# Kernel tuning notes

Measured on AMD Instinct MI355X. Metric: run time of the kernel, lower is better.

The kernel has to match this reference:

```python
import jax, jax.numpy as jnp
import numpy as np

N = 100000  # nodes
IN, HID, OUT = 64, 64, 32  # in_channels, 2*out_channels, out_channels
E = 1600000  # edges (avg degree 16)


def _gcn_conv(x, src, dst, deg_inv_sqrt, W, b, n):
    # PyG GCNConv: h = X W ; out[dst] += norm * h[src] ; out += b
    h = x @ W  # [N, F_out]
    norm = (deg_inv_sqrt[src] * deg_inv_sqrt[dst])[:, None]  # [E+N, 1]
    msg = h[src] * norm  # gathered edge messages [E+N, F_out]
    return jax.ops.segment_sum(msg, dst, num_segments=n) + b


def setup_inputs() -> dict:
    key = jax.random.key(0)
    ks = jax.random.split(key, 6)
    x = jax.random.normal(ks[0], (N, IN), dtype=jnp.float32)
    edge_index = jax.random.randint(ks[1], (2, E), 0, N, dtype=jnp.int32)
    # glorot-ish init for the two GCN layers
    W1 = jax.random.normal(ks[2], (IN, HID), dtype=jnp.float32) * (1.0 / np.sqrt(IN))
    b1 = jnp.zeros((HID,), dtype=jnp.float32)
    W2 = jax.random.normal(ks[3], (HID, OUT), dtype=jnp.float32) * (1.0 / np.sqrt(HID))
    b2 = jnp.zeros((OUT,), dtype=jnp.float32)
    return {"x": x, "edge_index": edge_index, "W1": W1, "b1": b1, "W2": W2, "b2": b2}


def reference(x, edge_index, W1, b1, W2, b2):
    n = x.shape[0]
    loop = jnp.arange(n, dtype=edge_index.dtype)
    src = jnp.concatenate([edge_index[0], loop])  # add self-loops
    dst = jnp.concatenate([edge_index[1], loop])
    # symmetric degree normalization (deg includes self-loops, so deg >= 1)
    deg = jax.ops.segment_sum(jnp.ones(dst.shape[0], x.dtype), dst, num_segments=n)
    dis = jax.lax.rsqrt(deg)
    h = jax.nn.relu(_gcn_conv(x, src, dst, dis, W1, b1, n))
    out = jax.nn.relu(_gcn_conv(h, src, dst, dis, W2, b2, n))
    return out
```

## Files before the change

### kernel.cpp

```cpp
#include <hip/hip_runtime.h>


#define NBMAX 512

__device__ __forceinline__ unsigned bf16pair(float a, float b) {
  unsigned ua = __float_as_uint(a), ub = __float_as_uint(b);
  ua = (ua + 0x7fffu + ((ua >> 16) & 1u)) >> 16;
  ub = (ub + 0x7fffu + ((ub >> 16) & 1u)) >> 16;
  return ua | (ub << 16);
}
__device__ __forceinline__ float bf_lo(unsigned v) { return __uint_as_float(v << 16); }
__device__ __forceinline__ float bf_hi(unsigned v) { return __uint_as_float(v & 0xffff0000u); }


__global__ __launch_bounds__(256) void k_coarsehist(const int* __restrict__ dst,
                                                    int* __restrict__ ch,
                                                    int E, int NB) {
  __shared__ int lh[NBMAX];
  int t = threadIdx.x;
  lh[t] = 0; lh[t + 256] = 0;
  __syncthreads();
  for (int e = blockIdx.x * 256 + t; e < E; e += gridDim.x * 256)
    atomicAdd(&lh[dst[e] >> 8], 1);
  __syncthreads();
  for (int b = t; b < NB; b += 256) {
    int c = lh[b];
    if (c) atomicAdd(&ch[b], c);
  }
}

__global__ __launch_bounds__(512) void k_scanb(const int* __restrict__ ch,
                                               int* __restrict__ cbase,
                                               int* __restrict__ gcur,
                                               int* __restrict__ off,
                                               int NB, int n, int E) {
  __shared__ int lds[512];
  int t = threadIdx.x;
  int v = (t < NB) ? ch[t] : 0;
  lds[t] = v;
  __syncthreads();
  for (int d = 1; d < 512; d <<= 1) {
    int u = (t >= d) ? lds[t - d] : 0;
    __syncthreads();
    lds[t] += u;
    __syncthreads();
  }
  if (t < NB) {
    int exc = lds[t] - v;
    cbase[t] = exc;
    gcur[t]  = exc;
  }
  if (t == 0) off[n] = E;
}

__global__ __launch_bounds__(256) void k_binpairs(const int* __restrict__ src,
                                                  const int* __restrict__ dst,
                                                  int* __restrict__ gcur,
                                                  unsigned* __restrict__ pairs,
                                                  int E, int NB) {
  __shared__ int lcnt[NBMAX], gbase[NBMAX];
  int t = threadIdx.x;
  int tile0 = blockIdx.x * 4096;
  lcnt[t] = 0; lcnt[t + 256] = 0;
  __syncthreads();
#pragma unroll
  for (int j = 0; j < 16; ++j) {
    int e = tile0 + j * 256 + t;
    if (e < E) atomicAdd(&lcnt[dst[e] >> 8], 1);
  }
  __syncthreads();
  for (int b = t; b < NB; b += 256) {
    int c = lcnt[b];
    if (c) gbase[b] = atomicAdd(&gcur[b], c);
    lcnt[b] = 0;
  }
  __syncthreads();
#pragma unroll
  for (int j = 0; j < 16; ++j) {
    int e = tile0 + j * 256 + t;
    if (e < E) {
      int dv = dst[e];
      int b  = dv >> 8;
      int slot = atomicAdd(&lcnt[b], 1);
      pairs[gbase[b] + slot] = ((unsigned)src[e] << 8) | (unsigned)(dv & 255);
    }
  }
}

__global__ __launch_bounds__(256) void k_finesort(const unsigned* __restrict__ pairs,
                                                  const int* __restrict__ ch,
                                                  const int* __restrict__ cbase,
                                                  int* __restrict__ off,
                                                  float* __restrict__ dis,
                                                  int* __restrict__ ssrc, int n) {
  __shared__ int hist[256], lcur[256], wsum[4];
  __shared__ int sbuf[8192];
  int b = blockIdx.x;
  int node0 = b << 8;
  int nn = min(256, n - node0);
  int cnt = ch[b], base = cbase[b];
  int t = threadIdx.x;
  hist[t] = 0;
  __syncthreads();
  for (int e = t; e < cnt; e += 256)
    atomicAdd(&hist[pairs[base + e] & 255u], 1);
  __syncthreads();
  int c = hist[t];
  int lane = t & 63, wv = t >> 6;
  int inc = c;
#pragma unroll
  for (int d = 1; d < 64; d <<= 1) {
    int u = __shfl_up(inc, d);
    if (lane >= d) inc += u;
  }
  if (lane == 63) wsum[wv] = inc;
  __syncthreads();
  int pre = 0;
  for (int w = 0; w < wv; ++w) pre += wsum[w];
  int exc = pre + inc - c;
  if (t < nn) {
    off[node0 + t] = base + exc;
    dis[node0 + t] = rsqrtf((float)(c + 1));
  }
  lcur[t] = exc;
  __syncthreads();
  bool inlds = (cnt <= 8192);
  for (int e = t; e < cnt; e += 256) {
    unsigned p = pairs[base + e];
    int slot = atomicAdd(&lcur[p & 255u], 1);
    int sv = (int)(p >> 8);
    if (inlds) sbuf[slot] = sv;
    else       ssrc[base + slot] = sv;
  }
  __syncthreads();
  if (inlds)
    for (int e = t; e < cnt; e += 256) ssrc[base + e] = sbuf[e];
}


__device__ __forceinline__ int swz(int r, int q) {
  return r * 16 + (q ^ ((r >> 3) & 7));
}

__global__ __launch_bounds__(128) void k_gemm64t(const float* __restrict__ X,
                                                 const float* __restrict__ W,
                                                 const float* __restrict__ dis,
                                                 unsigned* __restrict__ Hb, int n) {
  __shared__ float4 Xl[128 * 16];
  __shared__ float4 Wl[64 * 16];
  int t = threadIdx.x;
  int row0 = blockIdx.x * 128;
#pragma unroll
  for (int j = 0; j < 8; ++j) Wl[t + j * 128] = ((const float4*)W)[t + j * 128];
#pragma unroll
  for (int j = 0; j < 16; ++j) {
    int v = t + j * 128;
    int r = v >> 4, q = v & 15;
    int gr = row0 + r;
    float4 val = (gr < n) ? ((const float4*)X)[(size_t)gr * 16 + q]
                          : make_float4(0.f, 0.f, 0.f, 0.f);
    Xl[swz(r, q)] = val;
  }
  __syncthreads();
  int tx = t & 7, ty = t >> 3;
  float acc[8][8];
#pragma unroll
  for (int i = 0; i < 8; ++i)
#pragma unroll
    for (int j = 0; j < 8; ++j) acc[i][j] = 0.f;
  int tysw = ty & 7;
  for (int kq = 0; kq < 16; ++kq) {
    float x_[8][4];
#pragma unroll
    for (int i = 0; i < 8; ++i) {
      float4 v = Xl[(ty * 8 + i) * 16 + (kq ^ tysw)];
      x_[i][0] = v.x; x_[i][1] = v.y; x_[i][2] = v.z; x_[i][3] = v.w;
    }
#pragma unroll
    for (int kk = 0; kk < 4; ++kk) {
      int k = kq * 4 + kk;
      float4 w0 = Wl[k * 16 + tx * 2];
      float4 w1 = Wl[k * 16 + tx * 2 + 1];
      float w_[8] = {w0.x, w0.y, w0.z, w0.w, w1.x, w1.y, w1.z, w1.w};
#pragma unroll
      for (int i = 0; i < 8; ++i)
#pragma unroll
        for (int j = 0; j < 8; ++j)
          acc[i][j] = fmaf(x_[i][kk], w_[j], acc[i][j]);
    }
  }
#pragma unroll
  for (int i = 0; i < 8; ++i) {
    int r = row0 + ty * 8 + i;
    if (r < n) {
      float d = dis[r];
      uint4 o;
      o.x = bf16pair(acc[i][0] * d, acc[i][1] * d);
      o.y = bf16pair(acc[i][2] * d, acc[i][3] * d);
      o.z = bf16pair(acc[i][4] * d, acc[i][5] * d);
      o.w = bf16pair(acc[i][6] * d, acc[i][7] * d);
      ((uint4*)Hb)[(size_t)r * 8 + tx] = o;
    }
  }
}

__global__ __launch_bounds__(128) void k_gemm32t(const float* __restrict__ P,
                                                 const float* __restrict__ W2,
                                                 const float* __restrict__ dis,
                                                 unsigned* __restrict__ Hb, int n) {
  __shared__ float4 Pl[128 * 16];
  __shared__ float4 Wl[64 * 8];
  int t = threadIdx.x;
  int row0 = blockIdx.x * 128;
#pragma unroll
  for (int j = 0; j < 4; ++j) Wl[t + j * 128] = ((const float4*)W2)[t + j * 128];
#pragma unroll
  for (int j = 0; j < 16; ++j) {
    int v = t + j * 128;
    int r = v >> 4, q = v & 15;
    int gr = row0 + r;
    float4 val = (gr < n) ? ((const float4*)P)[(size_t)gr * 16 + q]
                          : make_float4(0.f, 0.f, 0.f, 0.f);
    Pl[swz(r, q)] = val;
  }
  __syncthreads();
  int tx = t & 7, ty = t >> 3;
  float acc[8][4];
#pragma unroll
  for (int i = 0; i < 8; ++i)
#pragma unroll
    for (int j = 0; j < 4; ++j) acc[i][j] = 0.f;
  int tysw = ty & 7;
  for (int kq = 0; kq < 16; ++kq) {
    float x_[8][4];
#pragma unroll
    for (int i = 0; i < 8; ++i) {
      float4 v = Pl[(ty * 8 + i) * 16 + (kq ^ tysw)];
      x_[i][0] = v.x; x_[i][1] = v.y; x_[i][2] = v.z; x_[i][3] = v.w;
    }
#pragma unroll
    for (int kk = 0; kk < 4; ++kk) {
      int k = kq * 4 + kk;
      float4 w = Wl[k * 8 + tx];
      float w_[4] = {w.x, w.y, w.z, w.w};
#pragma unroll
      for (int i = 0; i < 8; ++i)
#pragma unroll
        for (int j = 0; j < 4; ++j)
          acc[i][j] = fmaf(x_[i][kk], w_[j], acc[i][j]);
    }
  }
#pragma unroll
  for (int i = 0; i < 8; ++i) {
    int r = row0 + ty * 8 + i;
    if (r < n) {
      float d = dis[r];
      uint2 o;
      o.x = bf16pair(acc[i][0] * d, acc[i][1] * d);
      o.y = bf16pair(acc[i][2] * d, acc[i][3] * d);
      ((uint2*)Hb)[(size_t)r * 8 + tx] = o;
    }
  }
}


__global__ __launch_bounds__(256) void k_gather64v(const int* __restrict__ off,
                                                   const int* __restrict__ ssrc,
                                                   const float* __restrict__ dis,
                                                   const uint2* __restrict__ Hb2,
                                                   const float* __restrict__ b1,
                                                   float* __restrict__ P, int n) {
  int lane = threadIdx.x & 63;
  int q = lane & 15, g = lane >> 4;
  int i = blockIdx.x * 4 + (threadIdx.x >> 6);
  if (i >= n) return;
  int beg = off[i], end = off[i + 1];
  float s0 = 0.f, s1 = 0.f, s2 = 0.f, s3 = 0.f;
  if (g == 0) {
    uint2 v = Hb2[(size_t)i * 16 + q];
    s0 = bf_lo(v.x); s1 = bf_hi(v.x); s2 = bf_lo(v.y); s3 = bf_hi(v.y);
  }
  int e = beg + g;
  for (; e + 4 < end; e += 8) {
    uint2 v0 = Hb2[(size_t)ssrc[e] * 16 + q];
    uint2 v1 = Hb2[(size_t)ssrc[e + 4] * 16 + q];
    s0 += bf_lo(v0.x) + bf_lo(v1.x);
    s1 += bf_hi(v0.x) + bf_hi(v1.x);
    s2 += bf_lo(v0.y) + bf_lo(v1.y);
    s3 += bf_hi(v0.y) + bf_hi(v1.y);
  }
  for (; e < end; e += 4) {
    uint2 v = Hb2[(size_t)ssrc[e] * 16 + q];
    s0 += bf_lo(v.x); s1 += bf_hi(v.x); s2 += bf_lo(v.y); s3 += bf_hi(v.y);
  }
  s0 += __shfl_xor(s0, 16); s1 += __shfl_xor(s1, 16);
  s2 += __shfl_xor(s2, 16); s3 += __shfl_xor(s3, 16);
  s0 += __shfl_xor(s0, 32); s1 += __shfl_xor(s1, 32);
  s2 += __shfl_xor(s2, 32); s3 += __shfl_xor(s3, 32);
  if (lane < 16) {
    float di = dis[i];
    float4 b = ((const float4*)b1)[q];
    float4 o;
    o.x = fmaxf(fmaf(di, s0, b.x), 0.f);
    o.y = fmaxf(fmaf(di, s1, b.y), 0.f);
    o.z = fmaxf(fmaf(di, s2, b.z), 0.f);
    o.w = fmaxf(fmaf(di, s3, b.w), 0.f);
    ((float4*)P)[(size_t)i * 16 + q] = o;
  }
}

__global__ __launch_bounds__(256) void k_gather32v(const int* __restrict__ off,
                                                   const int* __restrict__ ssrc,
                                                   const float* __restrict__ dis,
                                                   const uint2* __restrict__ Hb2,
                                                   const float* __restrict__ b2,
                                                   float* __restrict__ out, int n) {
  int lane = threadIdx.x & 63;
  int q = lane & 7, g = lane >> 3;
  int i = blockIdx.x * 4 + (threadIdx.x >> 6);
  if (i >= n) return;
  int beg = off[i], end = off[i + 1];
  float s0 = 0.f, s1 = 0.f, s2 = 0.f, s3 = 0.f;
  if (g == 0) {
    uint2 v = Hb2[(size_t)i * 8 + q];
    s0 = bf_lo(v.x); s1 = bf_hi(v.x); s2 = bf_lo(v.y); s3 = bf_hi(v.y);
  }
  int e = beg + g;
  for (; e + 8 < end; e += 16) {
    uint2 v0 = Hb2[(size_t)ssrc[e] * 8 + q];
    uint2 v1 = Hb2[(size_t)ssrc[e + 8] * 8 + q];
    s0 += bf_lo(v0.x) + bf_lo(v1.x);
    s1 += bf_hi(v0.x) + bf_hi(v1.x);
    s2 += bf_lo(v0.y) + bf_lo(v1.y);
    s3 += bf_hi(v0.y) + bf_hi(v1.y);
  }
  for (; e < end; e += 8) {
    uint2 v = Hb2[(size_t)ssrc[e] * 8 + q];
    s0 += bf_lo(v.x); s1 += bf_hi(v.x); s2 += bf_lo(v.y); s3 += bf_hi(v.y);
  }
  s0 += __shfl_xor(s0, 8);  s1 += __shfl_xor(s1, 8);
  s2 += __shfl_xor(s2, 8);  s3 += __shfl_xor(s3, 8);
  s0 += __shfl_xor(s0, 16); s1 += __shfl_xor(s1, 16);
  s2 += __shfl_xor(s2, 16); s3 += __shfl_xor(s3, 16);
  s0 += __shfl_xor(s0, 32); s1 += __shfl_xor(s1, 32);
  s2 += __shfl_xor(s2, 32); s3 += __shfl_xor(s3, 32);
  if (lane < 8) {
    float di = dis[i];
    float4 b = ((const float4*)b2)[q];
    float4 o;
    o.x = fmaxf(fmaf(di, s0, b.x), 0.f);
    o.y = fmaxf(fmaf(di, s1, b.y), 0.f);
    o.z = fmaxf(fmaf(di, s2, b.z), 0.f);
    o.w = fmaxf(fmaf(di, s3, b.w), 0.f);
    ((float4*)out)[(size_t)i * 8 + q] = o;
  }
}

extern "C" void kernel_launch(void* const* d_in, const int* in_sizes, int n_in,
                              void* d_out, int out_size, void* d_ws, size_t ws_size,
                              hipStream_t stream) {
  const float* x  = (const float*)d_in[0];
  const int*   ei = (const int*)d_in[1];
  const float* W1 = (const float*)d_in[2];
  const float* b1 = (const float*)d_in[3];
  const float* W2 = (const float*)d_in[4];
  const float* b2 = (const float*)d_in[5];
  float* out = (float*)d_out;

  const int n = in_sizes[0] / 64;
  const int E = in_sizes[1] / 2;
  const int* src = ei;
  const int* dst = ei + E;
  const int NB = (n + 255) >> 8;

  char* wp = (char*)d_ws;
  auto alloc = [&](size_t bytes) {
    char* p = wp;
    wp += (bytes + 15) & ~(size_t)15;
    return (void*)p;
  };
  unsigned* pairs = (unsigned*)alloc((size_t)E * 4);
  int*      ch    = (int*)alloc(NBMAX * 4);
  int*      cbase = (int*)alloc(NBMAX * 4);
  int*      gcur  = (int*)alloc(NBMAX * 4);
  int*      off   = (int*)alloc(((size_t)n + 1) * 4);
  float*    dis   = (float*)alloc((size_t)n * 4);
  int*      ssrc  = (int*)alloc((size_t)E * 4);
  unsigned* h1b   = (unsigned*)alloc((size_t)n * 64 * 2);
  float*    p1    = (float*)alloc((size_t)n * 64 * 4);
  unsigned* h2b   = (unsigned*)alloc((size_t)n * 32 * 2);

  auto cdiv = [](long long a, long long b) { return (unsigned)((a + b - 1) / b); };
  dim3 B(256);

  hipMemsetAsync(ch, 0, (size_t)NBMAX * 4, stream);
  k_coarsehist<<<512, B, 0, stream>>>(dst, ch, E, NB);
  k_scanb     <<<1, 512, 0, stream>>>(ch, cbase, gcur, off, NB, n, E);
  k_binpairs  <<<cdiv(E, 4096), B, 0, stream>>>(src, dst, gcur, pairs, E, NB);
  k_finesort  <<<NB, B, 0, stream>>>(pairs, ch, cbase, off, dis, ssrc, n);

  k_gemm64t   <<<cdiv(n, 128), 128, 0, stream>>>(x, W1, dis, h1b, n);
  k_gather64v <<<cdiv(n, 4), B, 0, stream>>>(off, ssrc, dis, (const uint2*)h1b, b1, p1, n);
  k_gemm32t   <<<cdiv(n, 128), 128, 0, stream>>>(p1, W2, dis, h2b, n);
  k_gather32v <<<cdiv(n, 4), B, 0, stream>>>(off, ssrc, dis, (const uint2*)h2b, b2, out, n);
}
```

Before: 203.0 us.

## Fuse layer-1 aggregation with layer-2 GEMM and enlarge sort tiles

Merges the layer-1 gather kernel with the 64x32 GEMM. Each wavefront multiplies its aggregated, ReLU'd row by W2 held in registers and reduces across lanes with shuffles. This drops the fp32 intermediate P (write plus re-read, about 51 MB) and one kernel launch. It also doubles the binning tile to 8192 edges per block and runs the fine sort with 512 threads. The cost is extra registers and shuffle work in the gather, and __syncthreads calls now sit inside divergent branches of the fine sort.

Measured after the change: 262.1 us. 1.29x slower.

```diff
diff --git a/kernel.cpp b/kernel.cpp
--- a/kernel.cpp
+++ b/kernel.cpp
@@ -53,6 +53,7 @@
   if (t == 0) off[n] = E;
 }
 
+#define BIN_TILE 8192
 __global__ __launch_bounds__(256) void k_binpairs(const int* __restrict__ src,
                                                   const int* __restrict__ dst,
                                                   int* __restrict__ gcur,
@@ -60,11 +61,11 @@
                                                   int E, int NB) {
   __shared__ int lcnt[NBMAX], gbase[NBMAX];
   int t = threadIdx.x;
-  int tile0 = blockIdx.x * 4096;
+  int tile0 = blockIdx.x * BIN_TILE;
   lcnt[t] = 0; lcnt[t + 256] = 0;
   __syncthreads();
 #pragma unroll
-  for (int j = 0; j < 16; ++j) {
+  for (int j = 0; j < BIN_TILE / 256; ++j) {
     int e = tile0 + j * 256 + t;
     if (e < E) atomicAdd(&lcnt[dst[e] >> 8], 1);
   }
@@ -76,7 +77,7 @@
   }
   __syncthreads();
 #pragma unroll
-  for (int j = 0; j < 16; ++j) {
+  for (int j = 0; j < BIN_TILE / 256; ++j) {
     int e = tile0 + j * 256 + t;
     if (e < E) {
       int dv = dst[e];
@@ -87,7 +88,7 @@
   }
 }
 
-__global__ __launch_bounds__(256) void k_finesort(const unsigned* __restrict__ pairs,
+__global__ __launch_bounds__(512) void k_finesort(const unsigned* __restrict__ pairs,
                                                   const int* __restrict__ ch,
                                                   const int* __restrict__ cbase,
                                                   int* __restrict__ off,
@@ -100,32 +101,36 @@
   int nn = min(256, n - node0);
   int cnt = ch[b], base = cbase[b];
   int t = threadIdx.x;
-  hist[t] = 0;
-  __syncthreads();
-  for (int e = t; e < cnt; e += 256)
+  if (t < 256) hist[t] = 0;
+  __syncthreads();
+  for (int e = t; e < cnt; e += 512)
     atomicAdd(&hist[pairs[base + e] & 255u], 1);
   __syncthreads();
-  int c = hist[t];
-  int lane = t & 63, wv = t >> 6;
-  int inc = c;
-#pragma unroll
-  for (int d = 1; d < 64; d <<= 1) {
-    int u = __shfl_up(inc, d);
-    if (lane >= d) inc += u;
-  }
-  if (lane == 63) wsum[wv] = inc;
-  __syncthreads();
-  int pre = 0;
-  for (int w = 0; w < wv; ++w) pre += wsum[w];
-  int exc = pre + inc - c;
-  if (t < nn) {
-    off[node0 + t] = base + exc;
-    dis[node0 + t] = rsqrtf((float)(c + 1));
-  }
-  lcur[t] = exc;
+  if (t < 256) {
+    int c = hist[t];
+    int lane = t & 63, wv = t >> 6;
+    int inc = c;
+#pragma unroll
+    for (int d = 1; d < 64; d <<= 1) {
+      int u = __shfl_up(inc, d);
+      if (lane >= d) inc += u;
+    }
+    if (lane == 63) wsum[wv] = inc;
+    __syncthreads();
+    int pre = 0;
+    for (int w = 0; w < wv; ++w) pre += wsum[w];
+    int exc = pre + inc - c;
+    if (t < nn) {
+      off[node0 + t] = base + exc;
+      dis[node0 + t] = rsqrtf((float)(c + 1));
+    }
+    lcur[t] = exc;
+  } else {
+    __syncthreads();
+  }
   __syncthreads();
   bool inlds = (cnt <= 8192);
-  for (int e = t; e < cnt; e += 256) {
+  for (int e = t; e < cnt; e += 512) {
     unsigned p = pairs[base + e];
     int slot = atomicAdd(&lcur[p & 255u], 1);
     int sv = (int)(p >> 8);
@@ -134,7 +139,7 @@
   }
   __syncthreads();
   if (inlds)
-    for (int e = t; e < cnt; e += 256) ssrc[base + e] = sbuf[e];
+    for (int e = t; e < cnt; e += 512) ssrc[base + e] = sbuf[e];
 }
 
 
@@ -204,74 +209,23 @@
   }
 }
 
-__global__ __launch_bounds__(128) void k_gemm32t(const float* __restrict__ P,
-                                                 const float* __restrict__ W2,
-                                                 const float* __restrict__ dis,
-                                                 unsigned* __restrict__ Hb, int n) {
-  __shared__ float4 Pl[128 * 16];
-  __shared__ float4 Wl[64 * 8];
-  int t = threadIdx.x;
-  int row0 = blockIdx.x * 128;
-#pragma unroll
-  for (int j = 0; j < 4; ++j) Wl[t + j * 128] = ((const float4*)W2)[t + j * 128];
-#pragma unroll
-  for (int j = 0; j < 16; ++j) {
-    int v = t + j * 128;
-    int r = v >> 4, q = v & 15;
-    int gr = row0 + r;
-    float4 val = (gr < n) ? ((const float4*)P)[(size_t)gr * 16 + q]
-                          : make_float4(0.f, 0.f, 0.f, 0.f);
-    Pl[swz(r, q)] = val;
-  }
-  __syncthreads();
-  int tx = t & 7, ty = t >> 3;
-  float acc[8][4];
-#pragma unroll
-  for (int i = 0; i < 8; ++i)
-#pragma unroll
-    for (int j = 0; j < 4; ++j) acc[i][j] = 0.f;
-  int tysw = ty & 7;
-  for (int kq = 0; kq < 16; ++kq) {
-    float x_[8][4];
-#pragma unroll
-    for (int i = 0; i < 8; ++i) {
-      float4 v = Pl[(ty * 8 + i) * 16 + (kq ^ tysw)];
-      x_[i][0] = v.x; x_[i][1] = v.y; x_[i][2] = v.z; x_[i][3] = v.w;
-    }
-#pragma unroll
-    for (int kk = 0; kk < 4; ++kk) {
-      int k = kq * 4 + kk;
-      float4 w = Wl[k * 8 + tx];
-      float w_[4] = {w.x, w.y, w.z, w.w};
-#pragma unroll
-      for (int i = 0; i < 8; ++i)
-#pragma unroll
-        for (int j = 0; j < 4; ++j)
-          acc[i][j] = fmaf(x_[i][kk], w_[j], acc[i][j]);
-    }
-  }
-#pragma unroll
-  for (int i = 0; i < 8; ++i) {
-    int r = row0 + ty * 8 + i;
-    if (r < n) {
-      float d = dis[r];
-      uint2 o;
-      o.x = bf16pair(acc[i][0] * d, acc[i][1] * d);
-      o.y = bf16pair(acc[i][2] * d, acc[i][3] * d);
-      ((uint2*)Hb)[(size_t)r * 8 + tx] = o;
-    }
-  }
-}
-
-
-__global__ __launch_bounds__(256) void k_gather64v(const int* __restrict__ off,
-                                                   const int* __restrict__ ssrc,
-                                                   const float* __restrict__ dis,
-                                                   const uint2* __restrict__ Hb2,
-                                                   const float* __restrict__ b1,
-                                                   float* __restrict__ P, int n) {
+__global__ __launch_bounds__(256) void k_gathergemm(const int* __restrict__ off,
+                                                    const int* __restrict__ ssrc,
+                                                    const float* __restrict__ dis,
+                                                    const uint2* __restrict__ Hb2,
+                                                    const float* __restrict__ b1,
+                                                    const float* __restrict__ W2,
+                                                    unsigned* __restrict__ H2b, int n) {
   int lane = threadIdx.x & 63;
   int q = lane & 15, g = lane >> 4;
+  float w_[4][8];
+#pragma unroll
+  for (int m = 0; m < 4; ++m) {
+    const float4* wr = (const float4*)(W2 + (4 * q + m) * 32 + 8 * g);
+    float4 a = wr[0], b = wr[1];
+    w_[m][0] = a.x; w_[m][1] = a.y; w_[m][2] = a.z; w_[m][3] = a.w;
+    w_[m][4] = b.x; w_[m][5] = b.y; w_[m][6] = b.z; w_[m][7] = b.w;
+  }
   int i = blockIdx.x * 4 + (threadIdx.x >> 6);
   if (i >= n) return;
   int beg = off[i], end = off[i + 1];
@@ -282,7 +236,7 @@
   }
   int e = beg + g;
   for (; e + 4 < end; e += 8) {
-    uint2 v0 = Hb2[(size_t)ssrc[e] * 16 + q];
+    uint2 v0 = Hb2[(size_t)ssrc[e]     * 16 + q];
     uint2 v1 = Hb2[(size_t)ssrc[e + 4] * 16 + q];
     s0 += bf_lo(v0.x) + bf_lo(v1.x);
     s1 += bf_hi(v0.x) + bf_hi(v1.x);
@@ -297,17 +251,27 @@
   s2 += __shfl_xor(s2, 16); s3 += __shfl_xor(s3, 16);
   s0 += __shfl_xor(s0, 32); s1 += __shfl_xor(s1, 32);
   s2 += __shfl_xor(s2, 32); s3 += __shfl_xor(s3, 32);
-  if (lane < 16) {
-    float di = dis[i];
-    float4 b = ((const float4*)b1)[q];
-    float4 o;
-    o.x = fmaxf(fmaf(di, s0, b.x), 0.f);
-    o.y = fmaxf(fmaf(di, s1, b.y), 0.f);
-    o.z = fmaxf(fmaf(di, s2, b.z), 0.f);
-    o.w = fmaxf(fmaf(di, s3, b.w), 0.f);
-    ((float4*)P)[(size_t)i * 16 + q] = o;
-  }
-}
+  float di = dis[i];
+  float4 bb = ((const float4*)b1)[q];
+  float p0 = fmaxf(fmaf(di, s0, bb.x), 0.f);
+  float p1 = fmaxf(fmaf(di, s1, bb.y), 0.f);
+  float p2 = fmaxf(fmaf(di, s2, bb.z), 0.f);
+  float p3 = fmaxf(fmaf(di, s3, bb.w), 0.f);
+  float acc[8];
+#pragma unroll
+  for (int j = 0; j < 8; ++j)
+    acc[j] = fmaf(p0, w_[0][j], fmaf(p1, w_[1][j], fmaf(p2, w_[2][j], p3 * w_[3][j])));
+#pragma unroll
+  for (int d = 1; d < 16; d <<= 1) {
+#pragma unroll
+    for (int j = 0; j < 8; ++j) acc[j] += __shfl_xor(acc[j], d);
+  }
+  if (q < 4) {
+    unsigned o = bf16pair(di * acc[2 * q], di * acc[2 * q + 1]);
+    H2b[(size_t)i * 16 + g * 4 + q] = o;
+  }
+}
+
 
 __global__ __launch_bounds__(256) void k_gather32v(const int* __restrict__ off,
                                                    const int* __restrict__ ssrc,
@@ -327,7 +291,7 @@
   }
   int e = beg + g;
   for (; e + 8 < end; e += 16) {
-    uint2 v0 = Hb2[(size_t)ssrc[e] * 8 + q];
+    uint2 v0 = Hb2[(size_t)ssrc[e]     * 8 + q];
     uint2 v1 = Hb2[(size_t)ssrc[e + 8] * 8 + q];
     s0 += bf_lo(v0.x) + bf_lo(v1.x);
     s1 += bf_hi(v0.x) + bf_hi(v1.x);
@@ -387,7 +351,6 @@
   float*    dis   = (float*)alloc((size_t)n * 4);
   int*      ssrc  = (int*)alloc((size_t)E * 4);
   unsigned* h1b   = (unsigned*)alloc((size_t)n * 64 * 2);
-  float*    p1    = (float*)alloc((size_t)n * 64 * 4);
   unsigned* h2b   = (unsigned*)alloc((size_t)n * 32 * 2);
 
   auto cdiv = [](long long a, long long b) { return (unsigned)((a + b - 1) / b); };
@@ -396,11 +359,10 @@
   hipMemsetAsync(ch, 0, (size_t)NBMAX * 4, stream);
   k_coarsehist<<<512, B, 0, stream>>>(dst, ch, E, NB);
   k_scanb     <<<1, 512, 0, stream>>>(ch, cbase, gcur, off, NB, n, E);
-  k_binpairs  <<<cdiv(E, 4096), B, 0, stream>>>(src, dst, gcur, pairs, E, NB);
-  k_finesort  <<<NB, B, 0, stream>>>(pairs, ch, cbase, off, dis, ssrc, n);
+  k_binpairs  <<<cdiv(E, BIN_TILE), B, 0, stream>>>(src, dst, gcur, pairs, E, NB);
+  k_finesort  <<<NB, 512, 0, stream>>>(pairs, ch, cbase, off, dis, ssrc, n);
 
   k_gemm64t   <<<cdiv(n, 128), 128, 0, stream>>>(x, W1, dis, h1b, n);
-  k_gather64v <<<cdiv(n, 4), B, 0, stream>>>(off, ssrc, dis, (const uint2*)h1b, b1, p1, n);
-  k_gemm32t   <<<cdiv(n, 128), 128, 0, stream>>>(p1, W2, dis, h2b, n);
+  k_gathergemm<<<cdiv(n, 4), B, 0, stream>>>(off, ssrc, dis, (const uint2*)h1b, b1, W2, h2b, n);
   k_gather32v <<<cdiv(n, 4), B, 0, stream>>>(off, ssrc, dis, (const uint2*)h2b, b2, out, n);
 }
```

## Split layer-1 features into two 32-wide halves and gather each separately

Applied to the files above, without the earlier changes.

The first GEMM now writes its bf16 output as two separate 32-column arrays, and the layer-1 gather runs as two passes, one per half. Each pass reads 64-byte rows instead of 128-byte rows, which shrinks the random-gather working set so it fits better in cache, at the cost of reading the edge lists twice. The fine-sort kernel also moves to 512 threads per block, with the scan restricted to the first 256 threads. The bin tile size becomes a macro with an unchanged value.

Measured after the change: 224.1 us. 1.1x slower.

```diff
diff --git a/kernel.cpp b/kernel.cpp
--- a/kernel.cpp
+++ b/kernel.cpp
@@ -53,6 +53,7 @@
   if (t == 0) off[n] = E;
 }
 
+#define BIN_TILE 4096
 __global__ __launch_bounds__(256) void k_binpairs(const int* __restrict__ src,
                                                   const int* __restrict__ dst,
                                                   int* __restrict__ gcur,
@@ -60,11 +61,11 @@
                                                   int E, int NB) {
   __shared__ int lcnt[NBMAX], gbase[NBMAX];
   int t = threadIdx.x;
-  int tile0 = blockIdx.x * 4096;
+  int tile0 = blockIdx.x * BIN_TILE;
   lcnt[t] = 0; lcnt[t + 256] = 0;
   __syncthreads();
 #pragma unroll
-  for (int j = 0; j < 16; ++j) {
+  for (int j = 0; j < BIN_TILE / 256; ++j) {
     int e = tile0 + j * 256 + t;
     if (e < E) atomicAdd(&lcnt[dst[e] >> 8], 1);
   }
@@ -76,7 +77,7 @@
   }
   __syncthreads();
 #pragma unroll
-  for (int j = 0; j < 16; ++j) {
+  for (int j = 0; j < BIN_TILE / 256; ++j) {
     int e = tile0 + j * 256 + t;
     if (e < E) {
       int dv = dst[e];
@@ -87,7 +88,7 @@
   }
 }
 
-__global__ __launch_bounds__(256) void k_finesort(const unsigned* __restrict__ pairs,
+__global__ __launch_bounds__(512) void k_finesort(const unsigned* __restrict__ pairs,
                                                   const int* __restrict__ ch,
                                                   const int* __restrict__ cbase,
                                                   int* __restrict__ off,
@@ -100,32 +101,38 @@
   int nn = min(256, n - node0);
   int cnt = ch[b], base = cbase[b];
   int t = threadIdx.x;
-  hist[t] = 0;
-  __syncthreads();
-  for (int e = t; e < cnt; e += 256)
+  if (t < 256) hist[t] = 0;
+  __syncthreads();
+  for (int e = t; e < cnt; e += 512)
     atomicAdd(&hist[pairs[base + e] & 255u], 1);
   __syncthreads();
-  int c = hist[t];
-  int lane = t & 63, wv = t >> 6;
-  int inc = c;
-#pragma unroll
-  for (int d = 1; d < 64; d <<= 1) {
-    int u = __shfl_up(inc, d);
-    if (lane >= d) inc += u;
-  }
-  if (lane == 63) wsum[wv] = inc;
-  __syncthreads();
-  int pre = 0;
-  for (int w = 0; w < wv; ++w) pre += wsum[w];
-  int exc = pre + inc - c;
-  if (t < nn) {
-    off[node0 + t] = base + exc;
-    dis[node0 + t] = rsqrtf((float)(c + 1));
-  }
-  lcur[t] = exc;
+  int c = 0, inc = 0;
+  if (t < 256) {
+    c = hist[t];
+    int lane = t & 63;
+    inc = c;
+#pragma unroll
+    for (int d = 1; d < 64; d <<= 1) {
+      int u = __shfl_up(inc, d);
+      if (lane >= d) inc += u;
+    }
+    if (lane == 63) wsum[t >> 6] = inc;
+  }
+  __syncthreads();
+  if (t < 256) {
+    int wv = t >> 6;
+    int pre = 0;
+    for (int w = 0; w < wv; ++w) pre += wsum[w];
+    int exc = pre + inc - c;
+    if (t < nn) {
+      off[node0 + t] = base + exc;
+      dis[node0 + t] = rsqrtf((float)(c + 1));
+    }
+    lcur[t] = exc;
+  }
   __syncthreads();
   bool inlds = (cnt <= 8192);
-  for (int e = t; e < cnt; e += 256) {
+  for (int e = t; e < cnt; e += 512) {
     unsigned p = pairs[base + e];
     int slot = atomicAdd(&lcur[p & 255u], 1);
     int sv = (int)(p >> 8);
@@ -134,7 +141,7 @@
   }
   __syncthreads();
   if (inlds)
-    for (int e = t; e < cnt; e += 256) ssrc[base + e] = sbuf[e];
+    for (int e = t; e < cnt; e += 512) ssrc[base + e] = sbuf[e];
 }
 
 
@@ -145,7 +152,8 @@
 __global__ __launch_bounds__(128) void k_gemm64t(const float* __restrict__ X,
                                                  const float* __restrict__ W,
                                                  const float* __restrict__ dis,
-                                                 unsigned* __restrict__ Hb, int n) {
+                                                 unsigned* __restrict__ Hlo,
+                                                 unsigned* __restrict__ Hhi, int n) {
   __shared__ float4 Xl[128 * 16];
   __shared__ float4 Wl[64 * 16];
   int t = threadIdx.x;
@@ -189,6 +197,8 @@
           acc[i][j] = fmaf(x_[i][kk], w_[j], acc[i][j]);
     }
   }
+  unsigned* Hb = (tx < 4) ? Hlo : Hhi;
+  int txx = tx & 3;
 #pragma unroll
   for (int i = 0; i < 8; ++i) {
     int r = row0 + ty * 8 + i;
@@ -199,10 +209,58 @@
       o.y = bf16pair(acc[i][2] * d, acc[i][3] * d);
       o.z = bf16pair(acc[i][4] * d, acc[i][5] * d);
       o.w = bf16pair(acc[i][6] * d, acc[i][7] * d);
-      ((uint4*)Hb)[(size_t)r * 8 + tx] = o;
-    }
-  }
-}
+      ((uint4*)Hb)[(size_t)r * 4 + txx] = o;
+    }
+  }
+}
+
+__global__ __launch_bounds__(256) void k_gather64h(const int* __restrict__ off,
+                                                   const int* __restrict__ ssrc,
+                                                   const float* __restrict__ dis,
+                                                   const uint2* __restrict__ Hb2,
+                                                   const float* __restrict__ b1h,
+                                                   float4* __restrict__ P4, int n) {
+  int lane = threadIdx.x & 63;
+  int q = lane & 7, g = lane >> 3;
+  int i = blockIdx.x * 4 + (threadIdx.x >> 6);
+  if (i >= n) return;
+  int beg = off[i], end = off[i + 1];
+  float s0 = 0.f, s1 = 0.f, s2 = 0.f, s3 = 0.f;
+  if (g == 0) {
+    uint2 v = Hb2[(size_t)i * 8 + q];
+    s0 = bf_lo(v.x); s1 = bf_hi(v.x); s2 = bf_lo(v.y); s3 = bf_hi(v.y);
+  }
+  int e = beg + g;
+  for (; e + 8 < end; e += 16) {
+    uint2 v0 = Hb2[(size_t)ssrc[e]     * 8 + q];
+    uint2 v1 = Hb2[(size_t)ssrc[e + 8] * 8 + q];
+    s0 += bf_lo(v0.x) + bf_lo(v1.x);
+    s1 += bf_hi(v0.x) + bf_hi(v1.x);
+    s2 += bf_lo(v0.y) + bf_lo(v1.y);
+    s3 += bf_hi(v0.y) + bf_hi(v1.y);
+  }
+  for (; e < end; e += 8) {
+    uint2 v = Hb2[(size_t)ssrc[e] * 8 + q];
+    s0 += bf_lo(v.x); s1 += bf_hi(v.x); s2 += bf_lo(v.y); s3 += bf_hi(v.y);
+  }
+  s0 += __shfl_xor(s0, 8);  s1 += __shfl_xor(s1, 8);
+  s2 += __shfl_xor(s2, 8);  s3 += __shfl_xor(s3, 8);
+  s0 += __shfl_xor(s0, 16); s1 += __shfl_xor(s1, 16);
+  s2 += __shfl_xor(s2, 16); s3 += __shfl_xor(s3, 16);
+  s0 += __shfl_xor(s0, 32); s1 += __shfl_xor(s1, 32);
+  s2 += __shfl_xor(s2, 32); s3 += __shfl_xor(s3, 32);
+  if (lane < 8) {
+    float di = dis[i];
+    float4 b = ((const float4*)b1h)[q];
+    float4 o;
+    o.x = fmaxf(fmaf(di, s0, b.x), 0.f);
+    o.y = fmaxf(fmaf(di, s1, b.y), 0.f);
+    o.z = fmaxf(fmaf(di, s2, b.z), 0.f);
+    o.w = fmaxf(fmaf(di, s3, b.w), 0.f);
+    P4[(size_t)i * 16 + q] = o;
+  }
+}
+
 
 __global__ __launch_bounds__(128) void k_gemm32t(const float* __restrict__ P,
                                                  const float* __restrict__ W2,
@@ -263,51 +321,6 @@
   }
 }
 
-
-__global__ __launch_bounds__(256) void k_gather64v(const int* __restrict__ off,
-                                                   const int* __restrict__ ssrc,
-                                                   const float* __restrict__ dis,
-                                                   const uint2* __restrict__ Hb2,
-                                                   const float* __restrict__ b1,
-                                                   float* __restrict__ P, int n) {
-  int lane = threadIdx.x & 63;
-  int q = lane & 15, g = lane >> 4;
-  int i = blockIdx.x * 4 + (threadIdx.x >> 6);
-  if (i >= n) return;
-  int beg = off[i], end = off[i + 1];
-  float s0 = 0.f, s1 = 0.f, s2 = 0.f, s3 = 0.f;
-  if (g == 0) {
-    uint2 v = Hb2[(size_t)i * 16 + q];
-    s0 = bf_lo(v.x); s1 = bf_hi(v.x); s2 = bf_lo(v.y); s3 = bf_hi(v.y);
-  }
-  int e = beg + g;
-  for (; e + 4 < end; e += 8) {
-    uint2 v0 = Hb2[(size_t)ssrc[e] * 16 + q];
-    uint2 v1 = Hb2[(size_t)ssrc[e + 4] * 16 + q];
-    s0 += bf_lo(v0.x) + bf_lo(v1.x);
-    s1 += bf_hi(v0.x) + bf_hi(v1.x);
-    s2 += bf_lo(v0.y) + bf_lo(v1.y);
-    s3 += bf_hi(v0.y) + bf_hi(v1.y);
-  }
-  for (; e < end; e += 4) {
-    uint2 v = Hb2[(size_t)ssrc[e] * 16 + q];
-    s0 += bf_lo(v.x); s1 += bf_hi(v.x); s2 += bf_lo(v.y); s3 += bf_hi(v.y);
-  }
-  s0 += __shfl_xor(s0, 16); s1 += __shfl_xor(s1, 16);
-  s2 += __shfl_xor(s2, 16); s3 += __shfl_xor(s3, 16);
-  s0 += __shfl_xor(s0, 32); s1 += __shfl_xor(s1, 32);
-  s2 += __shfl_xor(s2, 32); s3 += __shfl_xor(s3, 32);
-  if (lane < 16) {
-    float di = dis[i];
-    float4 b = ((const float4*)b1)[q];
-    float4 o;
-    o.x = fmaxf(fmaf(di, s0, b.x), 0.f);
-    o.y = fmaxf(fmaf(di, s1, b.y), 0.f);
-    o.z = fmaxf(fmaf(di, s2, b.z), 0.f);
-    o.w = fmaxf(fmaf(di, s3, b.w), 0.f);
-    ((float4*)P)[(size_t)i * 16 + q] = o;
-  }
-}
 
 __global__ __launch_bounds__(256) void k_gather32v(const int* __restrict__ off,
                                                    const int* __restrict__ ssrc,
@@ -327,7 +340,7 @@
   }
   int e = beg + g;
   for (; e + 8 < end; e += 16) {
-    uint2 v0 = Hb2[(size_t)ssrc[e] * 8 + q];
+    uint2 v0 = Hb2[(size_t)ssrc[e]     * 8 + q];
     uint2 v1 = Hb2[(size_t)ssrc[e + 8] * 8 + q];
     s0 += bf_lo(v0.x) + bf_lo(v1.x);
     s1 += bf_hi(v0.x) + bf_hi(v1.x);
@@ -386,7 +399,8 @@
   int*      off   = (int*)alloc(((size_t)n + 1) * 4);
   float*    dis   = (float*)alloc((size_t)n * 4);
   int*      ssrc  = (int*)alloc((size_t)E * 4);
-  unsigned* h1b   = (unsigned*)alloc((size_t)n * 64 * 2);
+  unsigned* h1lo  = (unsigned*)alloc((size_t)n * 32 * 2);
+  unsigned* h1hi  = (unsigned*)alloc((size_t)n * 32 * 2);
   float*    p1    = (float*)alloc((size_t)n * 64 * 4);
   unsigned* h2b   = (unsigned*)alloc((size_t)n * 32 * 2);
 
@@ -396,11 +410,14 @@
   hipMemsetAsync(ch, 0, (size_t)NBMAX * 4, stream);
   k_coarsehist<<<512, B, 0, stream>>>(dst, ch, E, NB);
   k_scanb     <<<1, 512, 0, stream>>>(ch, cbase, gcur, off, NB, n, E);
-  k_binpairs  <<<cdiv(E, 4096), B, 0, stream>>>(src, dst, gcur, pairs, E, NB);
-  k_finesort  <<<NB, B, 0, stream>>>(pairs, ch, cbase, off, dis, ssrc, n);
-
-  k_gemm64t   <<<cdiv(n, 128), 128, 0, stream>>>(x, W1, dis, h1b, n);
-  k_gather64v <<<cdiv(n, 4), B, 0, stream>>>(off, ssrc, dis, (const uint2*)h1b, b1, p1, n);
+  k_binpairs  <<<cdiv(E, BIN_TILE), B, 0, stream>>>(src, dst, gcur, pairs, E, NB);
+  k_finesort  <<<NB, 512, 0, stream>>>(pairs, ch, cbase, off, dis, ssrc, n);
+
+  k_gemm64t   <<<cdiv(n, 128), 128, 0, stream>>>(x, W1, dis, h1lo, h1hi, n);
+  k_gather64h <<<cdiv(n, 4), B, 0, stream>>>(off, ssrc, dis, (const uint2*)h1lo,
+                                             b1,      (float4*)p1,     n);
+  k_gather64h <<<cdiv(n, 4), B, 0, stream>>>(off, ssrc, dis, (const uint2*)h1hi,
+                                             b1 + 32, (float4*)p1 + 8, n);
   k_gemm32t   <<<cdiv(n, 128), 128, 0, stream>>>(p1, W2, dis, h2b, n);
   k_gather32v <<<cdiv(n, 4), B, 0, stream>>>(off, ssrc, dis, (const uint2*)h2b, b2, out, n);
 }
```
